# Kernel tuning notes

Measured on AMD Instinct MI355X. Metric: run time of the kernel, lower is better.

Reference implementation:

```python
import jax, jax.numpy as jnp
from jax import lax
import numpy as np

B, N, CIN, COUT = 2, 4096, 64, 128
RADIUS = 0.15
K = int(16 * 1.5)
BN_EPS = 1e-5


def _conv1(x, w):  # 1x1 conv1d: x [B,C,N], w [O,C]
    return jnp.einsum('oc,bcn->bon', w, x)


def _conv2(x, w):  # 1x1 conv2d: x [B,C,N,K], w [O,C]
    return jnp.einsum('oc,bcnk->bonk', w, x)


def _bn(x, g, b):  # eval-mode BN with running_mean=0, running_var=1
    shp = (1, -1) + (1,) * (x.ndim - 2)
    scale = g / jnp.sqrt(1.0 + BN_EPS)
    return x * scale.reshape(shp) + b.reshape(shp)


def _ball_query(query, support, radius, k):
    # query [G,Q,3], support [G,S,3] -> idx [G,Q,k] (pointnet2 semantics:
    # first k in-radius support indices in order, padded with the first hit, 0 if none)
    q = lax.stop_gradient(query)
    s = lax.stop_gradient(support)
    d2 = (jnp.sum(q * q, -1)[:, :, None] + jnp.sum(s * s, -1)[:, None, :]
          - 2.0 * jnp.einsum('gqd,gsd->gqs', q, s))
    S = s.shape[1]
    score = jnp.where(d2 < radius * radius,
                      jnp.arange(S, dtype=jnp.int32)[None, None, :], jnp.int32(S))
    neg, idx = lax.top_k(-score, k)  # k smallest scores = first k hits
    valid = neg > -S
    first = jnp.where(valid[..., :1], idx[..., :1], 0)
    return jnp.where(valid, idx, first)


def _group(idx, support, query, feats):
    # support [G,S,3], query [G,Q,3], feats [G,C,S], idx [G,Q,k]
    gx = jax.vmap(lambda sp, ix: sp[ix])(support, idx)            # [G,Q,k,3]
    dp = jnp.transpose(gx - query[:, :, None, :], (0, 3, 1, 2))    # [G,3,Q,k]
    fj = jax.vmap(lambda fb, ix: fb[:, ix])(feats, idx)            # [G,C,Q,k]
    return dp, fj


def _fps_perm(pts):  # pts [K,3] -> FPS visiting order (permutation) [K] int32
    n = pts.shape[0]
    def step(carry, _):
        dists, last = carry
        d = jnp.sum((pts - pts[last]) ** 2, -1)
        dists = jnp.minimum(dists, d)
        nxt = jnp.argmax(dists).astype(jnp.int32)
        return (dists, nxt), nxt
    init = (jnp.full((n,), 1e10, pts.dtype), jnp.int32(0))
    _, rest = lax.scan(step, init, None, length=n - 1)
    return jnp.concatenate([jnp.zeros((1,), jnp.int32), rest])


def _forward(pc, f, pe_in, w1, g1, b1, wd1, gd1, bd1, wd2, gd2, bd2,
             wd3, gd3, bd3, ww, gw, bw, wc2, gc2, bc2):
    Bv, Nv, _ = pc.shape
    p = pc[..., :3]
    # convs1: conv1d + bn + relu
    f1 = jax.nn.relu(_bn(_conv1(f, w1), g1, b1))                   # [B,COUT,N]
    # main ball-query grouper (nsample=K)
    idx = _ball_query(p, p, RADIUS, K)                             # [B,N,K]
    dp, fj = _group(idx, p, p, f1)                                 # [B,3,N,K], [B,C,N,K]
    C = fj.shape[1]
    # torch .view(B*N, K, 3) on a contiguous [B,3,N,K] tensor (layout reinterpret,
    # replicated faithfully with reshape)
    new_dp = dp.reshape(Bv * Nv, K, 3)
    fidx = jax.vmap(_fps_perm)(lax.stop_gradient(new_dp))          # [B*N,K]
    new_dp = jnp.take_along_axis(new_dp, fidx[..., None], axis=1)
    new_dp = new_dp.reshape(Bv, 3, Nv, K)
    # deformable: 3->32->16->3, last block without activation
    h = jax.nn.relu(_bn(_conv2(new_dp, wd1), gd1, bd1))
    h = jax.nn.relu(_bn(_conv2(h, wd2), gd2, bd2))
    delta = _bn(_conv2(h, wd3), gd3, bd3)
    new_dp = new_dp + delta
    # np_assign: ball query with nsample=1 over each group of K points
    q2 = new_dp.reshape(Bv * Nv, K, 3)
    s2 = dp.reshape(Bv * Nv, K, 3)
    ft2 = fj.reshape(Bv * Nv, C, K)
    idx2 = _ball_query(q2, s2, RADIUS, 1)                          # [B*N,K,1]
    nn_dp, nn_fj = _group(idx2, s2, q2, ft2)                       # [B*N,3,K,1],[B*N,C,K,1]
    dp2 = nn_dp.reshape(Bv, 3, Nv, K)
    fj2 = nn_fj.reshape(Bv, C, Nv, K)
    # modulation weights + positional encoding
    mod = jax.nn.softmax(_bn(_conv2(fj2, ww), gw, bw), axis=-1)
    pe = jax.nn.relu(_bn(_conv2(dp2, wc2), gc2, bc2))
    fout = jnp.max((pe + fj2) * mod, axis=-1)                      # [B,COUT,N]
    return pc, fout, pe


def setup_inputs() -> dict:
    key = jax.random.key(0)
    ks = jax.random.split(key, 32)
    w = lambda k, o, i: jax.random.normal(k, (o, i), jnp.float32) * 0.05
    g = lambda k, c: jax.random.uniform(k, (c,), jnp.float32, 0.5, 1.5)
    b = lambda k, c: jax.random.normal(k, (c,), jnp.float32) * 0.05
    return {
        'pc': jax.random.uniform(ks[0], (B, N, 6), jnp.float32),
        'f': jax.random.normal(ks[1], (B, CIN, N), jnp.float32),
        'pe_in': jnp.zeros((B, 3, N), jnp.float32),
        'w1': w(ks[2], COUT, CIN), 'g1': g(ks[3], COUT), 'b1': b(ks[4], COUT),
        'wd1': w(ks[5], 32, 3), 'gd1': g(ks[6], 32), 'bd1': b(ks[7], 32),
        'wd2': w(ks[8], 16, 32), 'gd2': g(ks[9], 16), 'bd2': b(ks[10], 16),
        'wd3': w(ks[11], 3, 16), 'gd3': g(ks[12], 3), 'bd3': b(ks[13], 3),
        'ww': w(ks[14], COUT, COUT), 'gw': g(ks[15], COUT), 'bw': b(ks[16], COUT),
        'wc2': w(ks[17], COUT, 3), 'gc2': g(ks[18], COUT), 'bc2': b(ks[19], COUT),
    }


def reference(pc, f, pe_in, w1, g1, b1, wd1, gd1, bd1, wd2, gd2, bd2,
              wd3, gd3, bd3, ww, gw, bw, wc2, gc2, bc2):
    return _forward(pc, f, pe_in, w1, g1, b1, wd1, gd1, bd1, wd2, gd2, bd2,
                    wd3, gd3, bd3, ww, gw, bw, wc2, gc2, bc2)
```

## Files before the change

### kernel.cpp

```cpp
#include <hip/hip_runtime.h>
#include <stdint.h>


#define BB 2
#define NN 4096
#define CI 64
#define CO 128
#define KK 24
#define GQ (BB*NN)
#define NKK (NN*KK)

typedef __attribute__((ext_vector_type(8))) short short8;
typedef __attribute__((ext_vector_type(4))) float f32x4;

__device__ __forceinline__ float relu_(float x){ return fmaxf(x, 0.0f); }
__device__ __forceinline__ unsigned short f2bf(float x){
    unsigned int u = __float_as_uint(x);
    return (unsigned short)((u + 0x7FFFu + ((u>>16)&1u)) >> 16);
}

__global__ __launch_bounds__(256) void k_f1(const float* __restrict__ f, const float* __restrict__ w1,
                     const float* __restrict__ g1, const float* __restrict__ b1,
                     const float* __restrict__ pc, const float* __restrict__ ww,
                     float* __restrict__ f1T, float* __restrict__ outPc,
                     float* __restrict__ p, float* __restrict__ pS,
                     unsigned short* __restrict__ wwAbf)
{
    int tid = threadIdx.x;
    int bid = blockIdx.x;
    {
        int t = bid*256 + tid;
        if (t < BB*NN*6) {
            float v = pc[t];
            outPc[t] = v;
            int d = t % 6;
            if (d < 3) {
                int q = t/6;
                p[q*3 + d] = v;
                pS[d*GQ + q] = v;
            }
        }
        if (t < CO*CO) {
            int o = t >> 7, c = t & 127;
            int otile = o >> 4, m = o & 15;
            int ks = c >> 5, kk = c & 31;
            int lane = m | ((kk >> 3) << 4);
            int j = kk & 7;
            wwAbf[(((otile*4 + ks)*64 + lane)<<3) + j] = f2bf(ww[t]);
        }
    }
    __shared__ float W[CI*129];
    __shared__ float ft[CI*16];
    for (int i = tid; i < CI*CO; i += 256) {
        int o = i >> 6, c = i & 63;
        W[c*129 + o] = w1[i];
    }
    int b = bid >> 8;
    int n0 = (bid & 255) * 16;
    {
        int c = tid >> 2, nn = (tid & 3) * 4;
        float4 v = *(const float4*)(f + (size_t)b*CI*NN + (size_t)c*NN + n0 + nn);
        *(float4*)&ft[c*16 + nn] = v;
    }
    __syncthreads();
    int o = tid & 127, g = tid >> 7;
    float acc[8];
    #pragma unroll
    for (int j = 0; j < 8; ++j) acc[j] = 0.f;
    const float* ftg = ft + g*8;
    #pragma unroll 8
    for (int c = 0; c < CI; ++c) {
        float w = W[c*129 + o];
        float4 fa = *(const float4*)&ftg[c*16];
        float4 fb4 = *(const float4*)&ftg[c*16 + 4];
        acc[0] += w*fa.x;  acc[1] += w*fa.y;  acc[2] += w*fa.z;  acc[3] += w*fa.w;
        acc[4] += w*fb4.x; acc[5] += w*fb4.y; acc[6] += w*fb4.z; acc[7] += w*fb4.w;
    }
    float sc = g1[o] / sqrtf(1.00001f);
    float bo = b1[o];
    #pragma unroll
    for (int j = 0; j < 8; ++j) {
        int n = n0 + g*8 + j;
        f1T[((size_t)b*NN + n)*CO + o] = relu_(acc[j]*sc + bo);
    }
}

__global__ void k_bq1(const float* __restrict__ pS, int* __restrict__ idx)
{
    int wave = threadIdx.x >> 6;
    int lane = threadIdx.x & 63;
    int q = blockIdx.x*4 + wave;
    int b = q >> 12;
    int n = q & 4095;
    int boff = b << 12;
    const float* Sx = pS + boff;
    const float* Sy = pS + GQ + boff;
    const float* Sz = pS + 2*GQ + boff;
    float qx = Sx[n], qy = Sy[n], qz = Sz[n];
    float sq = qx*qx + qy*qy + qz*qz;
    const float rsq = (float)(0.15*0.15);
    int cnt = 0, first = 0;
    int* orow = idx + (size_t)q*KK;
    for (int chunk = 0; chunk < 64; ++chunk) {
        int s = chunk*64 + lane;
        float sx = Sx[s], sy = Sy[s], sz = Sz[s];
        float ss  = sx*sx + sy*sy + sz*sz;
        float dot = qx*sx + qy*sy + qz*sz;
        float d2 = (sq + ss) - 2.0f*dot;
        unsigned long long m = __ballot(d2 < rsq);
        while (m && cnt < KK) {
            int pos = __ffsll((unsigned long long)m) - 1;
            int sidx = chunk*64 + pos;
            if (cnt == 0) first = sidx;
            if (lane == 0) orow[cnt] = sidx;
            ++cnt;
            m &= m - 1;
        }
        if (cnt >= KK) break;
    }
    if (lane == 0)
        for (int j = cnt; j < KK; ++j) orow[j] = first;
}

__global__ __launch_bounds__(256) void k_geo(const float* __restrict__ p, const int* __restrict__ idx,
                                             float* __restrict__ dpf, float* __restrict__ ndp)
{
    int tid = threadIdx.x;
    int lane = tid & 31;
    int row = blockIdx.x*8 + (tid >> 5);
    float px = 0.f, py = 0.f, pz = 0.f, dist;
    if (lane < KK) {
        float v[3];
        #pragma unroll
        for (int d = 0; d < 3; ++d) {
            int u = 3*lane + d;
            int qq = u / 24;
            int kk = u - qq*24;
            int m = row*3 + qq;
            int b = (m >= 3*NN) ? 1 : 0;
            int rem = m - b*3*NN;
            int dd = rem >> 12;
            int n = rem & 4095;
            int base = (b << 12);
            int j = idx[((size_t)(base + n))*KK + kk];
            v[d] = p[(base + j)*3 + dd] - p[(base + n)*3 + dd];
        }
        px = v[0]; py = v[1]; pz = v[2];
        dist = 1e10f;
        float* drow = dpf + (size_t)row*72 + lane*3;
        drow[0] = px; drow[1] = py; drow[2] = pz;
    } else {
        dist = -3.4e38f;
    }
    float* dst = ndp + (size_t)row*72;
    if (lane == 0) { dst[0] = px; dst[1] = py; dst[2] = pz; }
    int last = 0;
    for (int j = 1; j < KK; ++j) {
        float lx = __shfl(px, last, 32);
        float ly = __shfl(py, last, 32);
        float lz = __shfl(pz, last, 32);
        float dx = px-lx, dy = py-ly, dz = pz-lz;
        float d = dx*dx + dy*dy + dz*dz;
        dist = fminf(dist, d);
        float val = dist; int idxl = lane;
        #pragma unroll
        for (int off = 16; off > 0; off >>= 1) {
            float ov = __shfl_xor(val, off, 32);
            int   oi = __shfl_xor(idxl, off, 32);
            if (ov > val || (ov == val && oi < idxl)) { val = ov; idxl = oi; }
        }
        if (lane == idxl) { dst[j*3+0] = px; dst[j*3+1] = py; dst[j*3+2] = pz; }
        last = idxl;
    }
}

__global__ void k_mlp(const float* __restrict__ ndp,
                      const float* __restrict__ wd1, const float* __restrict__ gd1, const float* __restrict__ bd1,
                      const float* __restrict__ wd2, const float* __restrict__ gd2, const float* __restrict__ bd2,
                      const float* __restrict__ wd3, const float* __restrict__ gd3, const float* __restrict__ bd3,
                      float* __restrict__ q2)
{
    __shared__ float W1[96], S1[32], B1s[32], W2[512], S2[16], B2s[16], W3[48], S3[3], B3s[3];
    int tid = threadIdx.x;
    const float inv = sqrtf(1.00001f);
    for (int i = tid; i < 96;  i += blockDim.x) W1[i]=wd1[i];
    for (int i = tid; i < 512; i += blockDim.x) W2[i]=wd2[i];
    for (int i = tid; i < 48;  i += blockDim.x) W3[i]=wd3[i];
    if (tid < 32) { S1[tid]=gd1[tid]/inv; B1s[tid]=bd1[tid]; }
    if (tid >= 32 && tid < 48) { int c=tid-32; S2[c]=gd2[c]/inv; B2s[c]=bd2[c]; }
    if (tid >= 48 && tid < 51) { int c=tid-48; S3[c]=gd3[c]/inv; B3s[c]=bd3[c]; }
    __syncthreads();
    int t = blockIdx.x*blockDim.x + tid;
    int k = t % KK, n = (t/KK)%NN, b = t/(NN*KK);
    size_t base = (((size_t)b*3)*NN + n)*KK + k;
    float x0 = ndp[base], x1 = ndp[base + NKK], x2 = ndp[base + 2*(size_t)NKK];
    float h1[32];
    #pragma unroll
    for (int o = 0; o < 32; ++o)
        h1[o] = relu_((W1[o*3+0]*x0 + W1[o*3+1]*x1 + W1[o*3+2]*x2)*S1[o] + B1s[o]);
    float h2[16];
    #pragma unroll
    for (int o = 0; o < 16; ++o) {
        float a = 0.f;
        #pragma unroll
        for (int c = 0; c < 32; ++c) a += W2[o*32+c]*h1[c];
        h2[o] = relu_(a*S2[o] + B2s[o]);
    }
    float xv[3] = {x0, x1, x2};
    #pragma unroll
    for (int d = 0; d < 3; ++d) {
        float a = 0.f;
        #pragma unroll
        for (int c = 0; c < 16; ++c) a += W3[d*16+c]*h2[c];
        q2[base + (size_t)d*NKK] = xv[d] + (a*S3[d] + B3s[d]);
    }
}

__global__ void k_bq2(const float* __restrict__ dpf, const float* __restrict__ q2f,
                      int* __restrict__ idx2, float* __restrict__ dp2)
{
    int t = blockIdx.x*blockDim.x + threadIdx.x;
    int g = t / KK, kq = t % KK;
    const float* srow = dpf + (size_t)g*72;
    const float* qp   = q2f + (size_t)g*72 + kq*3;
    float qx=qp[0], qy=qp[1], qz=qp[2];
    float sq = qx*qx + qy*qy + qz*qz;
    const float rsq = (float)(0.15*0.15);
    int j2 = 0;
    for (int s = 0; s < KK; ++s) {
        float sx=srow[s*3+0], sy=srow[s*3+1], sz=srow[s*3+2];
        float ss  = sx*sx + sy*sy + sz*sz;
        float dot = qx*sx + qy*sy + qz*sz;
        float d2 = (sq + ss) - 2.0f*dot;
        if (d2 < rsq) { j2 = s; break; }
    }
    idx2[t] = j2;
    float* drow = dp2 + (size_t)g*72;
    drow[0*KK + kq] = srow[j2*3+0] - qx;
    drow[1*KK + kq] = srow[j2*3+1] - qy;
    drow[2*KK + kq] = srow[j2*3+2] - qz;
}

__global__ __launch_bounds__(256, 4) void k_final(
    const float* __restrict__ f1T, const int* __restrict__ idx, const int* __restrict__ idx2,
    const float* __restrict__ dp2, const unsigned short* __restrict__ wwAbf,
    const float* __restrict__ gw, const float* __restrict__ bw,
    const float* __restrict__ wc2, const float* __restrict__ gc2, const float* __restrict__ bc2,
    float* __restrict__ fout, float* __restrict__ pe)
{
    __shared__ float GM[6400];
    __shared__ unsigned short Fbf[48*128];
    __shared__ float Ds[2][3][KK];
    __shared__ int   IRs[2][KK];
    int tid = threadIdx.x;
    int bid = blockIdx.x;
    int b = bid >> 11;
    int n0 = (bid & 2047)*2;

    if (tid < 48) {
        int nl = tid/24, kk = tid%24;
        IRs[nl][kk] = idx[((size_t)b*NN + (n0+nl))*KK + kk];
    }
    if (tid >= 64 && tid < 208) {
        int u = tid-64; int nl = u/72, r = u%72, d = r/24, k = r%24;
        Ds[nl][d][k] = dp2[(((size_t)b*3 + d)*NN + (n0+nl))*KK + k];
    }
    int c = tid & 127, kh = tid >> 7;
    int i2r[12];
    {
        int g = (b*CO + c)*32 + (n0 >> 7);
        const int4* i4 = (const int4*)(idx2 + (size_t)g*KK) + kh*3;
        int4 a = i4[0], bq = i4[1], cq4 = i4[2];
        i2r[0]=a.x; i2r[1]=a.y; i2r[2]=a.z; i2r[3]=a.w;
        i2r[4]=bq.x; i2r[5]=bq.y; i2r[6]=bq.z; i2r[7]=bq.w;
        i2r[8]=cq4.x; i2r[9]=cq4.y; i2r[10]=cq4.z; i2r[11]=cq4.w;
    }
    int wv = tid >> 6, l = tid & 63;
    const short8* wwA8 = (const short8*)wwAbf;
    short8 Af[2][4];
    #pragma unroll
    for (int ot = 0; ot < 2; ++ot)
        #pragma unroll
        for (int ks = 0; ks < 4; ++ks)
            Af[ot][ks] = wwA8[((wv*2 + ot)*4 + ks)*64 + l];
    __syncthreads();

    const float* basep = f1T + (size_t)b*NN*CO + c;
    #pragma unroll
    for (int nl = 0; nl < 2; ++nl)
        #pragma unroll
        for (int j = 0; j < 12; ++j) {
            int kk = kh*12 + j;
            GM[nl*3200 + c*25 + kk] = basep[(size_t)IRs[nl][kk]*CO];
        }
    __syncthreads();

    #pragma unroll
    for (int nl = 0; nl < 2; ++nl)
        #pragma unroll
        for (int j = 0; j < 12; ++j) {
            int col = nl*24 + kh*12 + j;
            unsigned int boff = (unsigned)((col*256 + c*2) ^ ((col&7)<<4));
            *(unsigned short*)((char*)Fbf + boff) = f2bf(GM[nl*3200 + c*25 + i2r[j]]);
        }
    __syncthreads();

    {
        f32x4 acc[2][3];
        #pragma unroll
        for (int ot=0;ot<2;++ot)
            #pragma unroll
            for (int ct=0;ct<3;++ct)
                acc[ot][ct] = (f32x4){0.f,0.f,0.f,0.f};
        int row_l = l & 15, kc_l = (l >> 4) << 3;
        #pragma unroll
        for (int ct = 0; ct < 3; ++ct) {
            int row = ct*16 + row_l;
            #pragma unroll
            for (int ks = 0; ks < 4; ++ks) {
                unsigned int boff = (unsigned)((row*256 + (ks*32 + kc_l)*2) ^ ((row&7)<<4));
                short8 Bf = *(const short8*)((const char*)Fbf + boff);
                acc[0][ct] = __builtin_amdgcn_mfma_f32_16x16x32_bf16(Af[0][ks], Bf, acc[0][ct], 0,0,0);
                acc[1][ct] = __builtin_amdgcn_mfma_f32_16x16x32_bf16(Af[1][ks], Bf, acc[1][ct], 0,0,0);
            }
        }
        #pragma unroll
        for (int ot = 0; ot < 2; ++ot) {
            int o = wv*32 + ot*16 + ((l>>4)<<2);
            #pragma unroll
            for (int ct = 0; ct < 3; ++ct) {
                int col = ct*16 + (l & 15);
                *(f32x4*)&GM[col*132 + o] = acc[ot][ct];
            }
        }
    }
    __syncthreads();

    int op = (tid & 127) >> 1, half = tid & 1, nl = tid >> 7;
    int k0 = half*12;
    int o0 = op*2;
    int n  = n0 + nl;
    int colb = nl*24 + k0;
    float a0[12], a1[12];
    #pragma unroll
    for (int j = 0; j < 12; ++j) {
        float2 m2 = *(const float2*)&GM[(colb+j)*132 + o0];
        a0[j] = m2.x; a1[j] = m2.y;
    }
    const float inv = sqrtf(1.00001f);
    float sw0 = gw[o0]/inv,   bw0 = bw[o0];
    float sw1 = gw[o0+1]/inv, bw1 = bw[o0+1];
    float pev0[12], pev1[12];
    {
        float wa0=wc2[o0*3], wa1=wc2[o0*3+1], wa2=wc2[o0*3+2];
        float wb0=wc2[o0*3+3], wb1=wc2[o0*3+4], wb2=wc2[o0*3+5];
        float sca = gc2[o0]/inv,   bca = bc2[o0];
        float scb = gc2[o0+1]/inv, bcb = bc2[o0+1];
        #pragma unroll
        for (int j = 0; j < 12; ++j) {
            float d0 = Ds[nl][0][k0+j], d1 = Ds[nl][1][k0+j], d2 = Ds[nl][2][k0+j];
            pev0[j] = relu_((wa0*d0 + wa1*d1 + wa2*d2)*sca + bca);
            pev1[j] = relu_((wb0*d0 + wb1*d1 + wb2*d2)*scb + bcb);
        }
    }
    float m0 = -3.4e38f, m1 = -3.4e38f;
    #pragma unroll
    for (int j=0;j<12;++j){
        a0[j] = a0[j]*sw0 + bw0; m0 = fmaxf(m0, a0[j]);
        a1[j] = a1[j]*sw1 + bw1; m1 = fmaxf(m1, a1[j]);
    }
    m0 = fmaxf(m0, __shfl_xor(m0, 1));
    m1 = fmaxf(m1, __shfl_xor(m1, 1));
    float s0 = 0.f, s1 = 0.f;
    #pragma unroll
    for (int j=0;j<12;++j){
        a0[j] = __expf(a0[j]-m0); s0 += a0[j];
        a1[j] = __expf(a1[j]-m1); s1 += a1[j];
    }
    s0 += __shfl_xor(s0, 1);
    s1 += __shfl_xor(s1, 1);
    float rs0 = 1.0f/s0, rs1 = 1.0f/s1;
    float fo0 = -3.4e38f, fo1 = -3.4e38f;
    #pragma unroll
    for (int j=0;j<12;++j){
        unsigned int boff = (unsigned)(((colb+j)*256 + o0*2) ^ (((colb+j)&7)<<4));
        unsigned int v = *(const unsigned int*)((const char*)Fbf + boff);
        float fj0 = __uint_as_float((v & 0xffffu) << 16);
        float fj1 = __uint_as_float((v >> 16) << 16);
        fo0 = fmaxf(fo0, (pev0[j] + fj0)*a0[j]*rs0);
        fo1 = fmaxf(fo1, (pev1[j] + fj1)*a1[j]*rs1);
    }
    fo0 = fmaxf(fo0, __shfl_xor(fo0, 1));
    fo1 = fmaxf(fo1, __shfl_xor(fo1, 1));
    fout[((size_t)b*CO + o0+half)*NN + n] = half ? fo1 : fo0;
    float* pr0 = pe + (((size_t)b*CO + o0)*NN + n)*KK + k0;
    float* pr1 = pe + (((size_t)b*CO + o0+1)*NN + n)*KK + k0;
    #pragma unroll
    for (int q4 = 0; q4 < 3; ++q4) {
        float4 v0, v1;
        v0.x=pev0[q4*4+0]; v0.y=pev0[q4*4+1]; v0.z=pev0[q4*4+2]; v0.w=pev0[q4*4+3];
        v1.x=pev1[q4*4+0]; v1.y=pev1[q4*4+1]; v1.z=pev1[q4*4+2]; v1.w=pev1[q4*4+3];
        ((float4*)pr0)[q4] = v0;
        ((float4*)pr1)[q4] = v1;
    }
}

extern "C" void kernel_launch(void* const* d_in, const int* in_sizes, int n_in,
                              void* d_out, int out_size, void* d_ws, size_t ws_size,
                              hipStream_t stream)
{
    const float* pc  = (const float*)d_in[0];
    const float* f   = (const float*)d_in[1];
    const float* w1  = (const float*)d_in[3];
    const float* g1  = (const float*)d_in[4];
    const float* b1  = (const float*)d_in[5];
    const float* wd1 = (const float*)d_in[6];
    const float* gd1 = (const float*)d_in[7];
    const float* bd1 = (const float*)d_in[8];
    const float* wd2 = (const float*)d_in[9];
    const float* gd2 = (const float*)d_in[10];
    const float* bd2 = (const float*)d_in[11];
    const float* wd3 = (const float*)d_in[12];
    const float* gd3 = (const float*)d_in[13];
    const float* bd3 = (const float*)d_in[14];
    const float* ww  = (const float*)d_in[15];
    const float* gw  = (const float*)d_in[16];
    const float* bw  = (const float*)d_in[17];
    const float* wc2 = (const float*)d_in[18];
    const float* gc2 = (const float*)d_in[19];
    const float* bc2 = (const float*)d_in[20];

    float* out     = (float*)d_out;
    float* outPc   = out;
    float* outFout = out + 49152;
    float* outPe   = out + 49152 + 1048576;

    char* ws = (char*)d_ws;
    size_t off = 0;
    auto alloc = [&](size_t bytes)->void* {
        void* q = ws + off; off += (bytes + 255) & ~(size_t)255; return q;
    };
    float* p    = (float*)alloc((size_t)GQ*3*4);
    float* pS   = (float*)alloc((size_t)GQ*3*4);
    float* f1T  = (float*)alloc((size_t)BB*NN*CO*4);
    int*   idx  = (int*)  alloc((size_t)BB*NN*KK*4);
    float* dpf  = (float*)alloc((size_t)BB*3*NN*KK*4);
    float* ndp  = (float*)alloc((size_t)BB*3*NN*KK*4);
    float* q2f  = (float*)alloc((size_t)BB*3*NN*KK*4);
    int*   idx2 = (int*)  alloc((size_t)GQ*KK*4);
    float* dp2  = (float*)alloc((size_t)GQ*72*4);
    unsigned short* wwAbf = (unsigned short*)alloc((size_t)CO*CO*2);

    k_f1   <<<dim3(512), dim3(256), 0, stream>>>(f, w1, g1, b1, pc, ww, f1T, outPc, p, pS, wwAbf);
    k_bq1  <<<dim3(GQ/4), dim3(256), 0, stream>>>(pS, idx);
    k_geo  <<<dim3(GQ/8), dim3(256), 0, stream>>>(p, idx, dpf, ndp);
    k_mlp  <<<dim3((BB*NN*KK)/256), dim3(256), 0, stream>>>(ndp, wd1,gd1,bd1, wd2,gd2,bd2, wd3,gd3,bd3, q2f);
    k_bq2  <<<dim3((GQ*KK)/256), dim3(256), 0, stream>>>(dpf, q2f, idx2, dp2);
    k_final<<<dim3(BB*NN/2), dim3(256), 0, stream>>>(f1T, idx, idx2, dp2, wwAbf, gw, bw, wc2, gc2, bc2, outFout, outPe);
}
```

Measured before the change: 121.9 us.

## Consume MFMA accumulators in registers and shrink LDS staging in final kernel

The final kernel now stores gathered features as bf16 in a smaller padded LDS buffer instead of a float matrix. It swaps the MFMA operand order so each lane holds one output channel across neighbours, and runs the softmax, max-pool and positional-encoding combine straight from the accumulators with cross-lane shuffles. This removes the LDS round trip of the GEMM result and one barrier. Lower LDS use and a raised occupancy hint allow more resident blocks, at the cost of more shuffles, extra positional-encoding recomputation and possible register pressure.

Result: slower. 134.2 us (+10.1%).

```diff
diff --git a/kernel.cpp b/kernel.cpp
--- a/kernel.cpp
+++ b/kernel.cpp
@@ -17,6 +17,9 @@
 __device__ __forceinline__ unsigned short f2bf(float x){
     unsigned int u = __float_as_uint(x);
     return (unsigned short)((u + 0x7FFFu + ((u>>16)&1u)) >> 16);
+}
+__device__ __forceinline__ float bfbits2f(unsigned short u){
+    return __uint_as_float(((unsigned int)u) << 16);
 }
 
 __global__ __launch_bounds__(256) void k_f1(const float* __restrict__ f, const float* __restrict__ w1,
@@ -241,14 +244,14 @@
     drow[2*KK + kq] = srow[j2*3+2] - qz;
 }
 
-__global__ __launch_bounds__(256, 4) void k_final(
+__global__ __launch_bounds__(256, 6) void k_final(
     const float* __restrict__ f1T, const int* __restrict__ idx, const int* __restrict__ idx2,
     const float* __restrict__ dp2, const unsigned short* __restrict__ wwAbf,
     const float* __restrict__ gw, const float* __restrict__ bw,
     const float* __restrict__ wc2, const float* __restrict__ gc2, const float* __restrict__ bc2,
     float* __restrict__ fout, float* __restrict__ pe)
 {
-    __shared__ float GM[6400];
+    __shared__ unsigned short Gs[2*128*26];
     __shared__ unsigned short Fbf[48*128];
     __shared__ float Ds[2][3][KK];
     __shared__ int   IRs[2][KK];
@@ -256,6 +259,7 @@
     int bid = blockIdx.x;
     int b = bid >> 11;
     int n0 = (bid & 2047)*2;
+    const float inv = sqrtf(1.00001f);
 
     if (tid < 48) {
         int nl = tid/24, kk = tid%24;
@@ -266,142 +270,161 @@
         Ds[nl][d][k] = dp2[(((size_t)b*3 + d)*NN + (n0+nl))*KK + k];
     }
     int c = tid & 127, kh = tid >> 7;
-    int i2r[12];
+    __syncthreads();
+
+    const float* basep = f1T + (size_t)b*NN*CO + c;
+    #pragma unroll
+    for (int nl = 0; nl < 2; ++nl)
+        #pragma unroll
+        for (int j = 0; j < 12; ++j) {
+            int kk = kh*12 + j;
+            Gs[nl*3328 + c*26 + kk] = f2bf(basep[(size_t)IRs[nl][kk]*CO]);
+        }
+    __syncthreads();
+
     {
         int g = (b*CO + c)*32 + (n0 >> 7);
         const int4* i4 = (const int4*)(idx2 + (size_t)g*KK) + kh*3;
-        int4 a = i4[0], bq = i4[1], cq4 = i4[2];
-        i2r[0]=a.x; i2r[1]=a.y; i2r[2]=a.z; i2r[3]=a.w;
-        i2r[4]=bq.x; i2r[5]=bq.y; i2r[6]=bq.z; i2r[7]=bq.w;
-        i2r[8]=cq4.x; i2r[9]=cq4.y; i2r[10]=cq4.z; i2r[11]=cq4.w;
-    }
-    int wv = tid >> 6, l = tid & 63;
-    const short8* wwA8 = (const short8*)wwAbf;
-    short8 Af[2][4];
-    #pragma unroll
-    for (int ot = 0; ot < 2; ++ot)
-        #pragma unroll
-        for (int ks = 0; ks < 4; ++ks)
-            Af[ot][ks] = wwA8[((wv*2 + ot)*4 + ks)*64 + l];
-    __syncthreads();
-
-    const float* basep = f1T + (size_t)b*NN*CO + c;
-    #pragma unroll
-    for (int nl = 0; nl < 2; ++nl)
-        #pragma unroll
-        for (int j = 0; j < 12; ++j) {
-            int kk = kh*12 + j;
-            GM[nl*3200 + c*25 + kk] = basep[(size_t)IRs[nl][kk]*CO];
-        }
-    __syncthreads();
-
-    #pragma unroll
-    for (int nl = 0; nl < 2; ++nl)
-        #pragma unroll
-        for (int j = 0; j < 12; ++j) {
-            int col = nl*24 + kh*12 + j;
-            unsigned int boff = (unsigned)((col*256 + c*2) ^ ((col&7)<<4));
-            *(unsigned short*)((char*)Fbf + boff) = f2bf(GM[nl*3200 + c*25 + i2r[j]]);
-        }
-    __syncthreads();
+        int4 ia = i4[0], ib = i4[1], ic = i4[2];
+        int i2r[12] = {ia.x,ia.y,ia.z,ia.w, ib.x,ib.y,ib.z,ib.w, ic.x,ic.y,ic.z,ic.w};
+        #pragma unroll
+        for (int nl = 0; nl < 2; ++nl)
+            #pragma unroll
+            for (int j = 0; j < 12; ++j) {
+                int col = nl*24 + kh*12 + j;
+                unsigned int boff = (unsigned)((col*256 + c*2) ^ ((col&7)<<4));
+                *(unsigned short*)((char*)Fbf + boff) = Gs[nl*3328 + c*26 + i2r[j]];
+            }
+    }
 
     {
-        f32x4 acc[2][3];
-        #pragma unroll
-        for (int ot=0;ot<2;++ot)
-            #pragma unroll
-            for (int ct=0;ct<3;++ct)
-                acc[ot][ct] = (f32x4){0.f,0.f,0.f,0.f};
-        int row_l = l & 15, kc_l = (l >> 4) << 3;
-        #pragma unroll
-        for (int ct = 0; ct < 3; ++ct) {
-            int row = ct*16 + row_l;
-            #pragma unroll
-            for (int ks = 0; ks < 4; ++ks) {
-                unsigned int boff = (unsigned)((row*256 + (ks*32 + kc_l)*2) ^ ((row&7)<<4));
-                short8 Bf = *(const short8*)((const char*)Fbf + boff);
-                acc[0][ct] = __builtin_amdgcn_mfma_f32_16x16x32_bf16(Af[0][ks], Bf, acc[0][ct], 0,0,0);
-                acc[1][ct] = __builtin_amdgcn_mfma_f32_16x16x32_bf16(Af[1][ks], Bf, acc[1][ct], 0,0,0);
-            }
-        }
-        #pragma unroll
-        for (int ot = 0; ot < 2; ++ot) {
-            int o = wv*32 + ot*16 + ((l>>4)<<2);
-            #pragma unroll
-            for (int ct = 0; ct < 3; ++ct) {
-                int col = ct*16 + (l & 15);
-                *(f32x4*)&GM[col*132 + o] = acc[ot][ct];
-            }
-        }
-    }
-    __syncthreads();
-
-    int op = (tid & 127) >> 1, half = tid & 1, nl = tid >> 7;
-    int k0 = half*12;
-    int o0 = op*2;
-    int n  = n0 + nl;
-    int colb = nl*24 + k0;
-    float a0[12], a1[12];
-    #pragma unroll
-    for (int j = 0; j < 12; ++j) {
-        float2 m2 = *(const float2*)&GM[(colb+j)*132 + o0];
-        a0[j] = m2.x; a1[j] = m2.y;
-    }
-    const float inv = sqrtf(1.00001f);
-    float sw0 = gw[o0]/inv,   bw0 = bw[o0];
-    float sw1 = gw[o0+1]/inv, bw1 = bw[o0+1];
-    float pev0[12], pev1[12];
-    {
+        int op = (tid & 127) >> 1, half = tid & 1, nl = tid >> 7;
+        int k0 = half*12, o0 = op*2, n = n0 + nl;
         float wa0=wc2[o0*3], wa1=wc2[o0*3+1], wa2=wc2[o0*3+2];
         float wb0=wc2[o0*3+3], wb1=wc2[o0*3+4], wb2=wc2[o0*3+5];
         float sca = gc2[o0]/inv,   bca = bc2[o0];
         float scb = gc2[o0+1]/inv, bcb = bc2[o0+1];
-        #pragma unroll
-        for (int j = 0; j < 12; ++j) {
-            float d0 = Ds[nl][0][k0+j], d1 = Ds[nl][1][k0+j], d2 = Ds[nl][2][k0+j];
-            pev0[j] = relu_((wa0*d0 + wa1*d1 + wa2*d2)*sca + bca);
-            pev1[j] = relu_((wb0*d0 + wb1*d1 + wb2*d2)*scb + bcb);
-        }
-    }
-    float m0 = -3.4e38f, m1 = -3.4e38f;
-    #pragma unroll
-    for (int j=0;j<12;++j){
-        a0[j] = a0[j]*sw0 + bw0; m0 = fmaxf(m0, a0[j]);
-        a1[j] = a1[j]*sw1 + bw1; m1 = fmaxf(m1, a1[j]);
-    }
-    m0 = fmaxf(m0, __shfl_xor(m0, 1));
-    m1 = fmaxf(m1, __shfl_xor(m1, 1));
-    float s0 = 0.f, s1 = 0.f;
-    #pragma unroll
-    for (int j=0;j<12;++j){
-        a0[j] = __expf(a0[j]-m0); s0 += a0[j];
-        a1[j] = __expf(a1[j]-m1); s1 += a1[j];
-    }
-    s0 += __shfl_xor(s0, 1);
-    s1 += __shfl_xor(s1, 1);
-    float rs0 = 1.0f/s0, rs1 = 1.0f/s1;
-    float fo0 = -3.4e38f, fo1 = -3.4e38f;
-    #pragma unroll
-    for (int j=0;j<12;++j){
-        unsigned int boff = (unsigned)(((colb+j)*256 + o0*2) ^ (((colb+j)&7)<<4));
-        unsigned int v = *(const unsigned int*)((const char*)Fbf + boff);
-        float fj0 = __uint_as_float((v & 0xffffu) << 16);
-        float fj1 = __uint_as_float((v >> 16) << 16);
-        fo0 = fmaxf(fo0, (pev0[j] + fj0)*a0[j]*rs0);
-        fo1 = fmaxf(fo1, (pev1[j] + fj1)*a1[j]*rs1);
-    }
-    fo0 = fmaxf(fo0, __shfl_xor(fo0, 1));
-    fo1 = fmaxf(fo1, __shfl_xor(fo1, 1));
-    fout[((size_t)b*CO + o0+half)*NN + n] = half ? fo1 : fo0;
-    float* pr0 = pe + (((size_t)b*CO + o0)*NN + n)*KK + k0;
-    float* pr1 = pe + (((size_t)b*CO + o0+1)*NN + n)*KK + k0;
-    #pragma unroll
-    for (int q4 = 0; q4 < 3; ++q4) {
-        float4 v0, v1;
-        v0.x=pev0[q4*4+0]; v0.y=pev0[q4*4+1]; v0.z=pev0[q4*4+2]; v0.w=pev0[q4*4+3];
-        v1.x=pev1[q4*4+0]; v1.y=pev1[q4*4+1]; v1.z=pev1[q4*4+2]; v1.w=pev1[q4*4+3];
-        ((float4*)pr0)[q4] = v0;
-        ((float4*)pr1)[q4] = v1;
+        float* pr0 = pe + (((size_t)b*CO + o0)*NN + n)*KK + k0;
+        float* pr1 = pe + (((size_t)b*CO + o0+1)*NN + n)*KK + k0;
+        #pragma unroll
+        for (int q4 = 0; q4 < 3; ++q4) {
+            float4 v0, v1;
+            #pragma unroll
+            for (int e = 0; e < 4; ++e) {
+                int k = k0 + q4*4 + e;
+                float d0 = Ds[nl][0][k], d1 = Ds[nl][1][k], d2 = Ds[nl][2][k];
+                float pa = relu_((wa0*d0 + wa1*d1 + wa2*d2)*sca + bca);
+                float pb = relu_((wb0*d0 + wb1*d1 + wb2*d2)*scb + bcb);
+                (&v0.x)[e] = pa; (&v1.x)[e] = pb;
+            }
+            ((float4*)pr0)[q4] = v0;
+            ((float4*)pr1)[q4] = v1;
+        }
+    }
+
+    int wv = tid >> 6, l = tid & 63;
+    const short8* wwA8 = (const short8*)wwAbf;
+    short8 Wf[2][4];
+    #pragma unroll
+    for (int ot = 0; ot < 2; ++ot)
+        #pragma unroll
+        for (int ks = 0; ks < 4; ++ks)
+            Wf[ot][ks] = wwA8[((wv*2 + ot)*4 + ks)*64 + l];
+    __syncthreads();
+
+    int l15 = l & 15, lh = l >> 4;
+    f32x4 acc[2][3];
+    #pragma unroll
+    for (int ot=0;ot<2;++ot)
+        #pragma unroll
+        for (int t=0;t<3;++t)
+            acc[ot][t] = (f32x4){0.f,0.f,0.f,0.f};
+    #pragma unroll
+    for (int t = 0; t < 3; ++t) {
+        int row = t*16 + l15;
+        #pragma unroll
+        for (int ks = 0; ks < 4; ++ks) {
+            unsigned int boff = (unsigned)((row*256 + (ks*32 + lh*8)*2) ^ ((row&7)<<4));
+            short8 Afr = *(const short8*)((const char*)Fbf + boff);
+            acc[0][t] = __builtin_amdgcn_mfma_f32_16x16x32_bf16(Afr, Wf[0][ks], acc[0][t], 0,0,0);
+            acc[1][t] = __builtin_amdgcn_mfma_f32_16x16x32_bf16(Afr, Wf[1][ks], acc[1][t], 0,0,0);
+        }
+    }
+
+    f32x4 Da[3], Db[3], Dc[3];
+    #pragma unroll
+    for (int d = 0; d < 3; ++d) {
+        Da[d] = *(const f32x4*)&Ds[0][d][4*lh];
+        Db[d] = (lh < 2) ? *(const f32x4*)&Ds[0][d][16 + 4*lh]
+                         : *(const f32x4*)&Ds[1][d][4*(lh-2)];
+        Dc[d] = *(const f32x4*)&Ds[1][d][8 + 4*lh];
+    }
+
+    #pragma unroll
+    for (int ot = 0; ot < 2; ++ot) {
+        int o = (2*wv + ot)*16 + l15;
+        float sw = gw[o]/inv, bwv = bw[o];
+        float L0[4], L1[4], L2[4];
+        #pragma unroll
+        for (int r=0;r<4;++r){
+            L0[r] = acc[ot][0][r]*sw + bwv;
+            L1[r] = acc[ot][1][r]*sw + bwv;
+            L2[r] = acc[ot][2][r]*sw + bwv;
+        }
+        float m0 = fmaxf(fmaxf(L0[0],L0[1]), fmaxf(L0[2],L0[3]));
+        float m1 = fmaxf(fmaxf(L2[0],L2[1]), fmaxf(L2[2],L2[3]));
+        float mt = fmaxf(fmaxf(L1[0],L1[1]), fmaxf(L1[2],L1[3]));
+        if (lh < 2) m0 = fmaxf(m0, mt); else m1 = fmaxf(m1, mt);
+        m0 = fmaxf(m0, __shfl_xor(m0, 16)); m0 = fmaxf(m0, __shfl_xor(m0, 32));
+        m1 = fmaxf(m1, __shfl_xor(m1, 16)); m1 = fmaxf(m1, __shfl_xor(m1, 32));
+        float mt1 = (lh < 2) ? m0 : m1;
+        float e0[4], e1[4], e2[4];
+        float s0 = 0.f, s1 = 0.f, st = 0.f;
+        #pragma unroll
+        for (int r=0;r<4;++r){
+            e0[r] = __expf(L0[r]-m0);  s0 += e0[r];
+            e2[r] = __expf(L2[r]-m1);  s1 += e2[r];
+            e1[r] = __expf(L1[r]-mt1); st += e1[r];
+        }
+        if (lh < 2) s0 += st; else s1 += st;
+        s0 += __shfl_xor(s0, 16); s0 += __shfl_xor(s0, 32);
+        s1 += __shfl_xor(s1, 16); s1 += __shfl_xor(s1, 32);
+        float rs0 = 1.0f/s0, rs1 = 1.0f/s1;
+        float rst = (lh < 2) ? rs0 : rs1;
+        float wa0=wc2[o*3], wa1=wc2[o*3+1], wa2=wc2[o*3+2];
+        float sca = gc2[o]/inv, bca = bc2[o];
+        float fo0 = -3.4e38f, fo1 = -3.4e38f;
+        #pragma unroll
+        for (int r=0;r<4;++r){
+            {
+                float pv = relu_((wa0*Da[0][r] + wa1*Da[1][r] + wa2*Da[2][r])*sca + bca);
+                int ci = 4*lh + r;
+                unsigned int boff = (unsigned)((ci*256 + o*2) ^ ((ci&7)<<4));
+                float fj = bfbits2f(*(const unsigned short*)((const char*)Fbf + boff));
+                fo0 = fmaxf(fo0, (pv + fj)*e0[r]*rs0);
+            }
+            {
+                float pv = relu_((wa0*Db[0][r] + wa1*Db[1][r] + wa2*Db[2][r])*sca + bca);
+                int ci = 16 + 4*lh + r;
+                unsigned int boff = (unsigned)((ci*256 + o*2) ^ ((ci&7)<<4));
+                float fj = bfbits2f(*(const unsigned short*)((const char*)Fbf + boff));
+                float v = (pv + fj)*e1[r]*rst;
+                if (lh < 2) fo0 = fmaxf(fo0, v); else fo1 = fmaxf(fo1, v);
+            }
+            {
+                float pv = relu_((wa0*Dc[0][r] + wa1*Dc[1][r] + wa2*Dc[2][r])*sca + bca);
+                int ci = 32 + 4*lh + r;
+                unsigned int boff = (unsigned)((ci*256 + o*2) ^ ((ci&7)<<4));
+                float fj = bfbits2f(*(const unsigned short*)((const char*)Fbf + boff));
+                fo1 = fmaxf(fo1, (pv + fj)*e2[r]*rs1);
+            }
+        }
+        fo0 = fmaxf(fo0, __shfl_xor(fo0, 16)); fo0 = fmaxf(fo0, __shfl_xor(fo0, 32));
+        fo1 = fmaxf(fo1, __shfl_xor(fo1, 16)); fo1 = fmaxf(fo1, __shfl_xor(fo1, 32));
+        if (lh == 0) {
+            float2 fv; fv.x = fo0; fv.y = fo1;
+            *(float2*)&fout[((size_t)b*CO + o)*NN + n0] = fv;
+        }
     }
 }
 
```
